# Kernel optimization log

Hardware: AMD Instinct MI355X
Metric: run time of the kernel (lower is better)

The kernel has to match this reference:

```python
import jax, jax.numpy as jnp
import numpy as np

NUM_GRAPHS = 512  # number of segments (graphs) in the batch


def setup_inputs() -> dict:
    key = jax.random.key(0)
    k1, k2, k3, k4, k5, k6 = jax.random.split(key, 6)
    N, Din, D, H = 100000, 1024, 64, 32
    x = jax.random.normal(k1, (N, Din), dtype=jnp.float32)
    batch = jnp.sort(jax.random.randint(k2, (N,), 0, NUM_GRAPHS)).astype(jnp.int64)
    W_enc = jax.random.normal(k3, (D, Din), dtype=jnp.float32) * (1.0 / np.sqrt(Din))
    b_enc = jax.random.normal(k4, (D,), dtype=jnp.float32) * 0.01
    W_gate = jax.random.normal(k5, (H, D), dtype=jnp.float32) * (1.0 / np.sqrt(D))
    b_gate = jax.random.normal(k6, (H,), dtype=jnp.float32) * 0.01
    return {"x": x, "batch": batch, "W_enc": W_enc, "b_enc": b_enc,
            "W_gate": W_gate, "b_gate": b_gate}


def reference(x, batch, W_enc, b_enc, W_gate, b_gate):
    B = NUM_GRAPHS
    batch = batch.astype(jnp.int32)
    # shared encoder: [N, Din] -> [N, D]
    xe = jnp.dot(x, W_enc.T) + b_enc
    # all 32 heads' scalar gates at once: [N, H]
    gate = jnp.dot(xe, W_gate.T) + b_gate
    # segment-wise (per-graph) stable softmax over nodes, per head
    gmax = jax.ops.segment_max(gate, batch, num_segments=B)          # [B, H]
    g = jnp.exp(gate - gmax[batch])                                   # [N, H]
    gsum = jax.ops.segment_sum(g, batch, num_segments=B)             # [B, H]
    alpha = g / gsum[batch]                                           # [N, H]
    # scatter-weighted sum: out[b,h,d] = sum_{n in graph b} alpha[n,h]*xe[n,d]
    weighted = alpha[:, :, None] * xe[:, None, :]                     # [N, H, D]
    pooled = jax.ops.segment_sum(weighted, batch, num_segments=B)    # [B, H, D]
    # concat over heads (head i occupies cols [i*D, (i+1)*D)) then ReLU
    return jax.nn.relu(pooled.reshape(B, -1))
```

## Files before the change

kernel.cpp:

```cpp
#include <hip/hip_runtime.h>


typedef short bf16x8 __attribute__((ext_vector_type(8)));
typedef float f32x4 __attribute__((ext_vector_type(4)));

#define NUM_GRAPHS 512
#define DIN 1024
#define DENC 64
#define NH 32
#define LDA 72
#define LDB 72

__device__ __forceinline__ unsigned short f2bf(float f) {
    unsigned int u = __float_as_uint(f);
    return (unsigned short)((u + 0x7fffu + ((u >> 16) & 1u)) >> 16);
}
__device__ __forceinline__ void split2(float f, unsigned short& h, unsigned short& l) {
    unsigned int u = __float_as_uint(f);
    unsigned int hb = (u + 0x7fffu + ((u >> 16) & 1u)) >> 16;
    h = (unsigned short)hb;
    float hf = __uint_as_float(hb << 16);
    l = f2bf(f - hf);
}

__device__ __forceinline__ int clampseg(int v) {
    return v < 0 ? 0 : (v >= NUM_GRAPHS ? NUM_GRAPHS - 1 : v);
}

__global__ void k_prep(const int* __restrict__ batch, int* __restrict__ seg, int N,
                       const float* __restrict__ W,
                       unsigned short* __restrict__ Wh,
                       unsigned short* __restrict__ Wl,
                       int nseg_blocks)
{
    const int blk = blockIdx.x;
    if (blk < nseg_blocks) {
        int n = blk * 256 + threadIdx.x;
        if (n >= N) return;
        int bc = clampseg(batch[n]);
        if (n == 0) {
            for (int j = 0; j <= bc; ++j) seg[j] = 0;
            int bl = clampseg(batch[N - 1]);
            for (int j = bl + 1; j <= NUM_GRAPHS; ++j) seg[j] = N;
        } else {
            int bp = clampseg(batch[n - 1]);
            for (int j = bp + 1; j <= bc; ++j) seg[j] = n;
        }
    } else {
        int idx = ((blk - nseg_blocks) * 256 + threadIdx.x) * 4;
        float4 v = *(const float4*)(W + idx);
        ushort4 h4, l4;
        split2(v.x, h4.x, l4.x);
        split2(v.y, h4.y, l4.y);
        split2(v.z, h4.z, l4.z);
        split2(v.w, h4.w, l4.w);
        *(ushort4*)(Wh + idx) = h4;
        *(ushort4*)(Wl + idx) = l4;
    }
}

__global__ __launch_bounds__(256, 2) void k_gemm(
    const float* __restrict__ x,
    const unsigned short* __restrict__ Wh,
    const unsigned short* __restrict__ Wl,
    const float* __restrict__ b_enc,
    float* __restrict__ xe,
    int N)
{
    __shared__ unsigned short Ah[128 * LDA], Al[128 * LDA];
    __shared__ unsigned short Bh[64 * LDB],  Bl[64 * LDB];

    const int tid  = threadIdx.x;
    const int lane = tid & 63;
    const int wv   = tid >> 6;
    const long brow = (long)blockIdx.x * 128;

    f32x4 acc[2][4];
    #pragma unroll
    for (int i = 0; i < 2; ++i)
        #pragma unroll
        for (int j = 0; j < 4; ++j) acc[i][j] = (f32x4){0.f, 0.f, 0.f, 0.f};

    const int ar0 = tid >> 4;
    const int ac4 = (tid & 15) * 4;
    const int br0 = tid >> 3;
    const int bc8 = (tid & 7) * 8;
    const int fr  = lane & 15;
    const int fq  = lane >> 4;

    float4 va[8];
    uint4  vbh[2], vbl[2];

    #pragma unroll
    for (int i = 0; i < 8; ++i) {
        int row = ar0 + 16 * i;
        long gr = brow + row;
        va[i] = (gr < N) ? *(const float4*)(x + gr * DIN + ac4)
                         : (float4){0.f, 0.f, 0.f, 0.f};
    }
    #pragma unroll
    for (int i = 0; i < 2; ++i) {
        int row = br0 + 32 * i;
        vbh[i] = *(const uint4*)(Wh + row * DIN + bc8);
        vbl[i] = *(const uint4*)(Wl + row * DIN + bc8);
    }

    for (int k0 = 0; k0 < DIN; k0 += 64) {
        #pragma unroll
        for (int i = 0; i < 8; ++i) {
            int row = ar0 + 16 * i;
            ushort4 h4, l4;
            split2(va[i].x, h4.x, l4.x);
            split2(va[i].y, h4.y, l4.y);
            split2(va[i].z, h4.z, l4.z);
            split2(va[i].w, h4.w, l4.w);
            *(ushort4*)&Ah[row * LDA + ac4] = h4;
            *(ushort4*)&Al[row * LDA + ac4] = l4;
        }
        #pragma unroll
        for (int i = 0; i < 2; ++i) {
            int row = br0 + 32 * i;
            *(uint4*)&Bh[row * LDB + bc8] = vbh[i];
            *(uint4*)&Bl[row * LDB + bc8] = vbl[i];
        }
        __syncthreads();

        const int kn = k0 + 64;
        if (kn < DIN) {
            #pragma unroll
            for (int i = 0; i < 8; ++i) {
                int row = ar0 + 16 * i;
                long gr = brow + row;
                va[i] = (gr < N) ? *(const float4*)(x + gr * DIN + kn + ac4)
                                 : (float4){0.f, 0.f, 0.f, 0.f};
            }
            #pragma unroll
            for (int i = 0; i < 2; ++i) {
                int row = br0 + 32 * i;
                vbh[i] = *(const uint4*)(Wh + row * DIN + kn + bc8);
                vbl[i] = *(const uint4*)(Wl + row * DIN + kn + bc8);
            }
        }

        #pragma unroll
        for (int kk = 0; kk < 64; kk += 32) {
            bf16x8 ah[2], al[2];
            #pragma unroll
            for (int rt = 0; rt < 2; ++rt) {
                int o = (wv * 32 + rt * 16 + fr) * LDA + fq * 8 + kk;
                ah[rt] = *(const bf16x8*)&Ah[o];
                al[rt] = *(const bf16x8*)&Al[o];
            }
            #pragma unroll
            for (int ct = 0; ct < 4; ++ct) {
                int o = (ct * 16 + fr) * LDB + fq * 8 + kk;
                bf16x8 bh = *(const bf16x8*)&Bh[o];
                bf16x8 bl = *(const bf16x8*)&Bl[o];
                #pragma unroll
                for (int rt = 0; rt < 2; ++rt) {
                    acc[rt][ct] = __builtin_amdgcn_mfma_f32_16x16x32_bf16(ah[rt], bh, acc[rt][ct], 0, 0, 0);
                    acc[rt][ct] = __builtin_amdgcn_mfma_f32_16x16x32_bf16(ah[rt], bl, acc[rt][ct], 0, 0, 0);
                    acc[rt][ct] = __builtin_amdgcn_mfma_f32_16x16x32_bf16(al[rt], bh, acc[rt][ct], 0, 0, 0);
                }
            }
        }
        __syncthreads();
    }

    float bv[4];
    #pragma unroll
    for (int ct = 0; ct < 4; ++ct) bv[ct] = b_enc[ct * 16 + fr];
    #pragma unroll
    for (int rt = 0; rt < 2; ++rt) {
        #pragma unroll
        for (int r = 0; r < 4; ++r) {
            long row = brow + wv * 32 + rt * 16 + fq * 4 + r;
            if (row < N) {
                float* o = xe + row * DENC;
                #pragma unroll
                for (int ct = 0; ct < 4; ++ct)
                    o[ct * 16 + fr] = acc[rt][ct][r] + bv[ct];
            }
        }
    }
}

__global__ __launch_bounds__(256) void k_gate(
    const float* __restrict__ xe,
    const float* __restrict__ Wg,
    const float* __restrict__ bg,
    float* __restrict__ gate,
    int N)
{
    __shared__ float xs[128 * 68];
    __shared__ float wgs[32 * 68];
    __shared__ float bgs[32];
    const int tid = threadIdx.x;
    const long brow = (long)blockIdx.x * 128;

    for (int i = tid; i < NH * DENC; i += 256) wgs[(i >> 6) * 68 + (i & 63)] = Wg[i];
    if (tid < NH) bgs[tid] = bg[tid];

    const int r0s = tid >> 4, c4 = (tid & 15) * 4;
    #pragma unroll
    for (int i = 0; i < 8; ++i) {
        int row = r0s + 16 * i;
        long gr = brow + row;
        if (gr < N)
            *(float4*)&xs[row * 68 + c4] = *(const float4*)(xe + gr * DENC + c4);
    }
    __syncthreads();

    const int r0 = tid & 31;
    const int h0 = (tid >> 5) * 4;
    float acc[4][4] = {};
    #pragma unroll
    for (int k = 0; k < 64; k += 4) {
        float4 w0 = *(const float4*)&wgs[(h0 + 0) * 68 + k];
        float4 w1 = *(const float4*)&wgs[(h0 + 1) * 68 + k];
        float4 w2 = *(const float4*)&wgs[(h0 + 2) * 68 + k];
        float4 w3 = *(const float4*)&wgs[(h0 + 3) * 68 + k];
        #pragma unroll
        for (int i = 0; i < 4; ++i) {
            float4 xv = *(const float4*)&xs[(r0 + 32 * i) * 68 + k];
            acc[i][0] += xv.x * w0.x + xv.y * w0.y + xv.z * w0.z + xv.w * w0.w;
            acc[i][1] += xv.x * w1.x + xv.y * w1.y + xv.z * w1.z + xv.w * w1.w;
            acc[i][2] += xv.x * w2.x + xv.y * w2.y + xv.z * w2.z + xv.w * w2.w;
            acc[i][3] += xv.x * w3.x + xv.y * w3.y + xv.z * w3.z + xv.w * w3.w;
        }
    }
    #pragma unroll
    for (int i = 0; i < 4; ++i) {
        long row = brow + r0 + 32 * i;
        if (row < N) {
            float4 o = { acc[i][0] + bgs[h0 + 0], acc[i][1] + bgs[h0 + 1],
                         acc[i][2] + bgs[h0 + 2], acc[i][3] + bgs[h0 + 3] };
            *(float4*)(gate + row * NH + h0) = o;
        }
    }
}

__global__ __launch_bounds__(256) void k_pool(
    const float* __restrict__ xe,
    const float* __restrict__ gate,
    const int* __restrict__ seg,
    float* __restrict__ out,
    int N)
{
    __shared__ float xs[64 * 68];
    __shared__ float gs[64 * 36];
    const int tid = threadIdx.x;
    const int b = blockIdx.x;
    const int s = seg[b], e = seg[b + 1];
    const long ob = (long)b * (NH * DENC);
    if (e <= s) {
        for (int i = tid; i < NH * DENC; i += 256) out[ob + i] = 0.f;
        return;
    }
    const int rl = tid & 63;
    const int hq = tid >> 6;
    const int h0 = hq * 8;
    const int r0s = tid >> 4, c4 = (tid & 15) * 4;

    float m[8], pool[8], gp[8];
    #pragma unroll
    for (int j = 0; j < 8; ++j) { m[j] = -INFINITY; pool[j] = 0.f; gp[j] = 0.f; }

    for (int base = s; base < e; base += 64) {
        const int nrow = min(64, e - base);
        #pragma unroll
        for (int i = 0; i < 4; ++i) {
            int row = r0s + 16 * i;
            if (row < nrow)
                *(float4*)&xs[row * 68 + c4] = *(const float4*)(xe + (long)(base + row) * DENC + c4);
        }
        float gv[8];
        const bool valid = (rl < nrow);
        if (valid) {
            const float* g0 = gate + (long)(base + rl) * NH + h0;
            float4 a = *(const float4*)g0;
            float4 c = *(const float4*)(g0 + 4);
            gv[0] = a.x; gv[1] = a.y; gv[2] = a.z; gv[3] = a.w;
            gv[4] = c.x; gv[5] = c.y; gv[6] = c.z; gv[7] = c.w;
        } else {
            #pragma unroll
            for (int j = 0; j < 8; ++j) gv[j] = -INFINITY;
        }
        float cm[8];
        #pragma unroll
        for (int j = 0; j < 8; ++j) cm[j] = gv[j];
        #pragma unroll
        for (int off = 32; off > 0; off >>= 1)
            #pragma unroll
            for (int j = 0; j < 8; ++j) cm[j] = fmaxf(cm[j], __shfl_xor(cm[j], off));
        #pragma unroll
        for (int j = 0; j < 8; ++j) {
            if (cm[j] > m[j]) {
                float sc = (m[j] == -INFINITY) ? 0.f : __expf(m[j] - cm[j]);
                pool[j] *= sc;
                gp[j]   *= sc;
                m[j] = cm[j];
            }
        }
        float4 ga = {0.f, 0.f, 0.f, 0.f}, gb = {0.f, 0.f, 0.f, 0.f};
        if (valid) {
            ga.x = __expf(gv[0] - m[0]); ga.y = __expf(gv[1] - m[1]);
            ga.z = __expf(gv[2] - m[2]); ga.w = __expf(gv[3] - m[3]);
            gb.x = __expf(gv[4] - m[4]); gb.y = __expf(gv[5] - m[5]);
            gb.z = __expf(gv[6] - m[6]); gb.w = __expf(gv[7] - m[7]);
            gp[0] += ga.x; gp[1] += ga.y; gp[2] += ga.z; gp[3] += ga.w;
            gp[4] += gb.x; gp[5] += gb.y; gp[6] += gb.z; gp[7] += gb.w;
        }
        *(float4*)&gs[rl * 36 + h0] = ga;
        *(float4*)&gs[rl * 36 + h0 + 4] = gb;
        __syncthreads();
        #pragma unroll 4
        for (int r2 = 0; r2 < nrow; ++r2) {
            float xv = xs[r2 * 68 + rl];
            float4 g1 = *(const float4*)&gs[r2 * 36 + h0];
            float4 g2 = *(const float4*)&gs[r2 * 36 + h0 + 4];
            pool[0] += g1.x * xv; pool[1] += g1.y * xv;
            pool[2] += g1.z * xv; pool[3] += g1.w * xv;
            pool[4] += g2.x * xv; pool[5] += g2.y * xv;
            pool[6] += g2.z * xv; pool[7] += g2.w * xv;
        }
        __syncthreads();
    }
    #pragma unroll
    for (int off = 32; off > 0; off >>= 1)
        #pragma unroll
        for (int j = 0; j < 8; ++j) gp[j] += __shfl_xor(gp[j], off);
    #pragma unroll
    for (int j = 0; j < 8; ++j) {
        float v = pool[j] / gp[j];
        out[ob + (h0 + j) * DENC + rl] = fmaxf(v, 0.f);
    }
}

extern "C" void kernel_launch(void* const* d_in, const int* in_sizes, int n_in,
                              void* d_out, int out_size, void* d_ws, size_t ws_size,
                              hipStream_t stream)
{
    const float* x      = (const float*)d_in[0];
    const int* batch    = (const int*)d_in[1];
    const float* W_enc  = (const float*)d_in[2];
    const float* b_enc  = (const float*)d_in[3];
    const float* W_gate = (const float*)d_in[4];
    const float* b_gate = (const float*)d_in[5];
    float* out = (float*)d_out;
    const int N = in_sizes[1];

    char* ws = (char*)d_ws;
    size_t off = 0;
    auto take = [&](size_t bytes) {
        char* p = ws + off;
        off += (bytes + 255) & ~(size_t)255;
        return p;
    };
    float* xe  = (float*)take((size_t)N * DENC * sizeof(float));
    float* gate = (float*)take((size_t)N * NH * sizeof(float));
    unsigned short* Wh = (unsigned short*)take((size_t)DENC * DIN * 2);
    unsigned short* Wl = (unsigned short*)take((size_t)DENC * DIN * 2);
    int* seg = (int*)take((NUM_GRAPHS + 1) * sizeof(int));
    (void)ws_size; (void)n_in; (void)out_size;

    const int nseg_blocks = (N + 255) / 256;
    const int nconv_blocks = (DENC * DIN) / 1024;
    k_prep<<<nseg_blocks + nconv_blocks, 256, 0, stream>>>(batch, seg, N, W_enc, Wh, Wl, nseg_blocks);
    k_gemm<<<(N + 127) / 128, 256, 0, stream>>>(x, Wh, Wl, b_enc, xe, N);
    k_gate<<<(N + 127) / 128, 256, 0, stream>>>(xe, W_gate, b_gate, gate, N);
    k_pool<<<NUM_GRAPHS, 256, 0, stream>>>(xe, gate, seg, out, N);
}
```

Baseline: 643.3 us.

## Fold gate projection into encoder GEMM via precomputed W_gate·W_enc, prefetch pool chunks

Precomputes a combined weight W_gate·W_enc and bias in the prep kernel and appends it as 32 extra output columns of the encoder GEMM, so gates come straight from x and the separate gate kernel disappears. This removes one launch plus the extra read of xe and write pass, at the cost of 50% more MFMA work and B-tile traffic per GEMM block, and slightly different rounding of the gate values. The pool kernel also prefetches the next chunk of xe and gate into registers before the barrier to overlap global loads with compute.

Result: no change. 632.1 us (-1.7%).

```diff
diff --git a/kernel.cpp b/kernel.cpp
--- a/kernel.cpp
+++ b/kernel.cpp
@@ -8,6 +8,7 @@
 #define DIN 1024
 #define DENC 64
 #define NH 32
+#define NB 96
 #define LDA 72
 #define LDB 72
 
@@ -29,13 +30,18 @@
 
 __global__ void k_prep(const int* __restrict__ batch, int* __restrict__ seg, int N,
                        const float* __restrict__ W,
+                       const float* __restrict__ Wg,
+                       const float* __restrict__ bg,
+                       const float* __restrict__ be,
                        unsigned short* __restrict__ Wh,
                        unsigned short* __restrict__ Wl,
-                       int nseg_blocks)
+                       float* __restrict__ bcomb,
+                       int nseg_blocks, int nconv_blocks)
 {
     const int blk = blockIdx.x;
+    const int tid = threadIdx.x;
     if (blk < nseg_blocks) {
-        int n = blk * 256 + threadIdx.x;
+        int n = blk * 256 + tid;
         if (n >= N) return;
         int bc = clampseg(batch[n]);
         if (n == 0) {
@@ -46,8 +52,8 @@
             int bp = clampseg(batch[n - 1]);
             for (int j = bp + 1; j <= bc; ++j) seg[j] = n;
         }
-    } else {
-        int idx = ((blk - nseg_blocks) * 256 + threadIdx.x) * 4;
+    } else if (blk < nseg_blocks + nconv_blocks) {
+        int idx = ((blk - nseg_blocks) * 256 + tid) * 4;
         float4 v = *(const float4*)(W + idx);
         ushort4 h4, l4;
         split2(v.x, h4.x, l4.x);
@@ -56,6 +62,30 @@
         split2(v.w, h4.w, l4.w);
         *(ushort4*)(Wh + idx) = h4;
         *(ushort4*)(Wl + idx) = l4;
+    } else {
+        __shared__ float wgr[DENC];
+        const int j = blk - nseg_blocks - nconv_blocks;
+        if (tid < DENC) wgr[tid] = Wg[j * DENC + tid];
+        __syncthreads();
+        const int k0 = tid * 4;
+        float4 a = {0.f, 0.f, 0.f, 0.f};
+        for (int d = 0; d < DENC; ++d) {
+            float w = wgr[d];
+            float4 v = *(const float4*)(W + d * DIN + k0);
+            a.x += w * v.x; a.y += w * v.y; a.z += w * v.z; a.w += w * v.w;
+        }
+        ushort4 h4, l4;
+        split2(a.x, h4.x, l4.x);
+        split2(a.y, h4.y, l4.y);
+        split2(a.z, h4.z, l4.z);
+        split2(a.w, h4.w, l4.w);
+        *(ushort4*)(Wh + (DENC + j) * DIN + k0) = h4;
+        *(ushort4*)(Wl + (DENC + j) * DIN + k0) = l4;
+        if (tid == 0) {
+            float s = bg[j];
+            for (int d = 0; d < DENC; ++d) s += wgr[d] * be[d];
+            bcomb[j] = s;
+        }
     }
 }
 
@@ -64,22 +94,24 @@
     const unsigned short* __restrict__ Wh,
     const unsigned short* __restrict__ Wl,
     const float* __restrict__ b_enc,
+    const float* __restrict__ bcomb,
     float* __restrict__ xe,
+    float* __restrict__ gate,
     int N)
 {
     __shared__ unsigned short Ah[128 * LDA], Al[128 * LDA];
-    __shared__ unsigned short Bh[64 * LDB],  Bl[64 * LDB];
+    __shared__ unsigned short Bh[NB * LDB],  Bl[NB * LDB];
 
     const int tid  = threadIdx.x;
     const int lane = tid & 63;
     const int wv   = tid >> 6;
     const long brow = (long)blockIdx.x * 128;
 
-    f32x4 acc[2][4];
+    f32x4 acc[2][6];
     #pragma unroll
     for (int i = 0; i < 2; ++i)
         #pragma unroll
-        for (int j = 0; j < 4; ++j) acc[i][j] = (f32x4){0.f, 0.f, 0.f, 0.f};
+        for (int j = 0; j < 6; ++j) acc[i][j] = (f32x4){0.f, 0.f, 0.f, 0.f};
 
     const int ar0 = tid >> 4;
     const int ac4 = (tid & 15) * 4;
@@ -89,7 +121,7 @@
     const int fq  = lane >> 4;
 
     float4 va[8];
-    uint4  vbh[2], vbl[2];
+    uint4  vbh[3], vbl[3];
 
     #pragma unroll
     for (int i = 0; i < 8; ++i) {
@@ -99,7 +131,7 @@
                          : (float4){0.f, 0.f, 0.f, 0.f};
     }
     #pragma unroll
-    for (int i = 0; i < 2; ++i) {
+    for (int i = 0; i < 3; ++i) {
         int row = br0 + 32 * i;
         vbh[i] = *(const uint4*)(Wh + row * DIN + bc8);
         vbl[i] = *(const uint4*)(Wl + row * DIN + bc8);
@@ -118,7 +150,7 @@
             *(ushort4*)&Al[row * LDA + ac4] = l4;
         }
         #pragma unroll
-        for (int i = 0; i < 2; ++i) {
+        for (int i = 0; i < 3; ++i) {
             int row = br0 + 32 * i;
             *(uint4*)&Bh[row * LDB + bc8] = vbh[i];
             *(uint4*)&Bl[row * LDB + bc8] = vbl[i];
@@ -135,7 +167,7 @@
                                  : (float4){0.f, 0.f, 0.f, 0.f};
             }
             #pragma unroll
-            for (int i = 0; i < 2; ++i) {
+            for (int i = 0; i < 3; ++i) {
                 int row = br0 + 32 * i;
                 vbh[i] = *(const uint4*)(Wh + row * DIN + kn + bc8);
                 vbl[i] = *(const uint4*)(Wl + row * DIN + kn + bc8);
@@ -152,7 +184,7 @@
                 al[rt] = *(const bf16x8*)&Al[o];
             }
             #pragma unroll
-            for (int ct = 0; ct < 4; ++ct) {
+            for (int ct = 0; ct < 6; ++ct) {
                 int o = (ct * 16 + fr) * LDB + fq * 8 + kk;
                 bf16x8 bh = *(const bf16x8*)&Bh[o];
                 bf16x8 bl = *(const bf16x8*)&Bl[o];
@@ -167,9 +199,11 @@
         __syncthreads();
     }
 
-    float bv[4];
+    float bv[4], bcv[2];
     #pragma unroll
     for (int ct = 0; ct < 4; ++ct) bv[ct] = b_enc[ct * 16 + fr];
+    #pragma unroll
+    for (int j = 0; j < 2; ++j) bcv[j] = bcomb[j * 16 + fr];
     #pragma unroll
     for (int rt = 0; rt < 2; ++rt) {
         #pragma unroll
@@ -180,62 +214,11 @@
                 #pragma unroll
                 for (int ct = 0; ct < 4; ++ct)
                     o[ct * 16 + fr] = acc[rt][ct][r] + bv[ct];
-            }
-        }
-    }
-}
-
-__global__ __launch_bounds__(256) void k_gate(
-    const float* __restrict__ xe,
-    const float* __restrict__ Wg,
-    const float* __restrict__ bg,
-    float* __restrict__ gate,
-    int N)
-{
-    __shared__ float xs[128 * 68];
-    __shared__ float wgs[32 * 68];
-    __shared__ float bgs[32];
-    const int tid = threadIdx.x;
-    const long brow = (long)blockIdx.x * 128;
-
-    for (int i = tid; i < NH * DENC; i += 256) wgs[(i >> 6) * 68 + (i & 63)] = Wg[i];
-    if (tid < NH) bgs[tid] = bg[tid];
-
-    const int r0s = tid >> 4, c4 = (tid & 15) * 4;
-    #pragma unroll
-    for (int i = 0; i < 8; ++i) {
-        int row = r0s + 16 * i;
-        long gr = brow + row;
-        if (gr < N)
-            *(float4*)&xs[row * 68 + c4] = *(const float4*)(xe + gr * DENC + c4);
-    }
-    __syncthreads();
-
-    const int r0 = tid & 31;
-    const int h0 = (tid >> 5) * 4;
-    float acc[4][4] = {};
-    #pragma unroll
-    for (int k = 0; k < 64; k += 4) {
-        float4 w0 = *(const float4*)&wgs[(h0 + 0) * 68 + k];
-        float4 w1 = *(const float4*)&wgs[(h0 + 1) * 68 + k];
-        float4 w2 = *(const float4*)&wgs[(h0 + 2) * 68 + k];
-        float4 w3 = *(const float4*)&wgs[(h0 + 3) * 68 + k];
-        #pragma unroll
-        for (int i = 0; i < 4; ++i) {
-            float4 xv = *(const float4*)&xs[(r0 + 32 * i) * 68 + k];
-            acc[i][0] += xv.x * w0.x + xv.y * w0.y + xv.z * w0.z + xv.w * w0.w;
-            acc[i][1] += xv.x * w1.x + xv.y * w1.y + xv.z * w1.z + xv.w * w1.w;
-            acc[i][2] += xv.x * w2.x + xv.y * w2.y + xv.z * w2.z + xv.w * w2.w;
-            acc[i][3] += xv.x * w3.x + xv.y * w3.y + xv.z * w3.z + xv.w * w3.w;
-        }
-    }
-    #pragma unroll
-    for (int i = 0; i < 4; ++i) {
-        long row = brow + r0 + 32 * i;
-        if (row < N) {
-            float4 o = { acc[i][0] + bgs[h0 + 0], acc[i][1] + bgs[h0 + 1],
-                         acc[i][2] + bgs[h0 + 2], acc[i][3] + bgs[h0 + 3] };
-            *(float4*)(gate + row * NH + h0) = o;
+                float* g = gate + row * NH;
+                #pragma unroll
+                for (int j = 0; j < 2; ++j)
+                    g[j * 16 + fr] = acc[rt][4 + j][r] + bcv[j];
+            }
         }
     }
 }
@@ -266,17 +249,17 @@
     #pragma unroll
     for (int j = 0; j < 8; ++j) { m[j] = -INFINITY; pool[j] = 0.f; gp[j] = 0.f; }
 
-    for (int base = s; base < e; base += 64) {
-        const int nrow = min(64, e - base);
+    float4 xv[4];
+    float gv[8];
+    auto load_chunk = [&](int base, int nrow) {
         #pragma unroll
         for (int i = 0; i < 4; ++i) {
             int row = r0s + 16 * i;
-            if (row < nrow)
-                *(float4*)&xs[row * 68 + c4] = *(const float4*)(xe + (long)(base + row) * DENC + c4);
-        }
-        float gv[8];
-        const bool valid = (rl < nrow);
-        if (valid) {
+            xv[i] = (row < nrow)
+                  ? *(const float4*)(xe + (long)(base + row) * DENC + c4)
+                  : (float4){0.f, 0.f, 0.f, 0.f};
+        }
+        if (rl < nrow) {
             const float* g0 = gate + (long)(base + rl) * NH + h0;
             float4 a = *(const float4*)g0;
             float4 c = *(const float4*)(g0 + 4);
@@ -286,6 +269,12 @@
             #pragma unroll
             for (int j = 0; j < 8; ++j) gv[j] = -INFINITY;
         }
+    };
+
+    load_chunk(s, min(64, e - s));
+
+    for (int base = s; base < e; base += 64) {
+        const int nrow = min(64, e - base);
         float cm[8];
         #pragma unroll
         for (int j = 0; j < 8; ++j) cm[j] = gv[j];
@@ -302,27 +291,30 @@
                 m[j] = cm[j];
             }
         }
-        float4 ga = {0.f, 0.f, 0.f, 0.f}, gb = {0.f, 0.f, 0.f, 0.f};
-        if (valid) {
-            ga.x = __expf(gv[0] - m[0]); ga.y = __expf(gv[1] - m[1]);
-            ga.z = __expf(gv[2] - m[2]); ga.w = __expf(gv[3] - m[3]);
-            gb.x = __expf(gv[4] - m[4]); gb.y = __expf(gv[5] - m[5]);
-            gb.z = __expf(gv[6] - m[6]); gb.w = __expf(gv[7] - m[7]);
-            gp[0] += ga.x; gp[1] += ga.y; gp[2] += ga.z; gp[3] += ga.w;
-            gp[4] += gb.x; gp[5] += gb.y; gp[6] += gb.z; gp[7] += gb.w;
-        }
+        float4 ga, gb;
+        ga.x = __expf(gv[0] - m[0]); ga.y = __expf(gv[1] - m[1]);
+        ga.z = __expf(gv[2] - m[2]); ga.w = __expf(gv[3] - m[3]);
+        gb.x = __expf(gv[4] - m[4]); gb.y = __expf(gv[5] - m[5]);
+        gb.z = __expf(gv[6] - m[6]); gb.w = __expf(gv[7] - m[7]);
+        gp[0] += ga.x; gp[1] += ga.y; gp[2] += ga.z; gp[3] += ga.w;
+        gp[4] += gb.x; gp[5] += gb.y; gp[6] += gb.z; gp[7] += gb.w;
+        #pragma unroll
+        for (int i = 0; i < 4; ++i)
+            *(float4*)&xs[(r0s + 16 * i) * 68 + c4] = xv[i];
         *(float4*)&gs[rl * 36 + h0] = ga;
         *(float4*)&gs[rl * 36 + h0 + 4] = gb;
+        int nb = base + 64;
+        if (nb < e) load_chunk(nb, min(64, e - nb));
         __syncthreads();
         #pragma unroll 4
         for (int r2 = 0; r2 < nrow; ++r2) {
-            float xv = xs[r2 * 68 + rl];
+            float xvv = xs[r2 * 68 + rl];
             float4 g1 = *(const float4*)&gs[r2 * 36 + h0];
             float4 g2 = *(const float4*)&gs[r2 * 36 + h0 + 4];
-            pool[0] += g1.x * xv; pool[1] += g1.y * xv;
-            pool[2] += g1.z * xv; pool[3] += g1.w * xv;
-            pool[4] += g2.x * xv; pool[5] += g2.y * xv;
-            pool[6] += g2.z * xv; pool[7] += g2.w * xv;
+            pool[0] += g1.x * xvv; pool[1] += g1.y * xvv;
+            pool[2] += g1.z * xvv; pool[3] += g1.w * xvv;
+            pool[4] += g2.x * xvv; pool[5] += g2.y * xvv;
+            pool[6] += g2.z * xvv; pool[7] += g2.w * xvv;
         }
         __syncthreads();
     }
@@ -357,17 +349,18 @@
         off += (bytes + 255) & ~(size_t)255;
         return p;
     };
-    float* xe  = (float*)take((size_t)N * DENC * sizeof(float));
+    float* xe   = (float*)take((size_t)N * DENC * sizeof(float));
     float* gate = (float*)take((size_t)N * NH * sizeof(float));
-    unsigned short* Wh = (unsigned short*)take((size_t)DENC * DIN * 2);
-    unsigned short* Wl = (unsigned short*)take((size_t)DENC * DIN * 2);
+    unsigned short* Wh = (unsigned short*)take((size_t)NB * DIN * 2);
+    unsigned short* Wl = (unsigned short*)take((size_t)NB * DIN * 2);
+    float* bcomb = (float*)take(NH * sizeof(float));
     int* seg = (int*)take((NUM_GRAPHS + 1) * sizeof(int));
     (void)ws_size; (void)n_in; (void)out_size;
 
-    const int nseg_blocks = (N + 255) / 256;
+    const int nseg_blocks  = (N + 255) / 256;
     const int nconv_blocks = (DENC * DIN) / 1024;
-    k_prep<<<nseg_blocks + nconv_blocks, 256, 0, stream>>>(batch, seg, N, W_enc, Wh, Wl, nseg_blocks);
-    k_gemm<<<(N + 127) / 128, 256, 0, stream>>>(x, Wh, Wl, b_enc, xe, N);
-    k_gate<<<(N + 127) / 128, 256, 0, stream>>>(xe, W_gate, b_gate, gate, N);
+    k_prep<<<nseg_blocks + nconv_blocks + NH, 256, 0, stream>>>(
+        batch, seg, N, W_enc, W_gate, b_gate, b_enc, Wh, Wl, bcomb, nseg_blocks, nconv_blocks);
+    k_gemm<<<(N + 127) / 128, 256, 0, stream>>>(x, Wh, Wl, b_enc, bcomb, xe, gate, N);
     k_pool<<<NUM_GRAPHS, 256, 0, stream>>>(xe, gate, seg, out, N);
 }
```
